# Optimization experiments

Measured on AMD Instinct MI355X. Metric: run time of the kernel, lower is better.

## Reference

```python
import jax, jax.numpy as jnp
import numpy as np

DIM = 2048
N_HEADS = 32
N_KV_HEADS = 8
HEAD_DIM = DIM // N_HEADS  # 64
N_REP = N_HEADS // N_KV_HEADS  # 4
BSZ = 2
SEQ = 2048


def setup_inputs() -> dict:
    key = jax.random.key(0)
    ks = jax.random.split(key, 7)
    s = 0.02
    return {
        "x": jax.random.normal(ks[0], (BSZ, SEQ, DIM), dtype=jnp.float32),
        "freqs_cos": jnp.cos(jnp.outer(jnp.arange(SEQ, dtype=jnp.float32),
                                       1.0 / (10000.0 ** (jnp.arange(0, HEAD_DIM, 2, dtype=jnp.float32) / HEAD_DIM)))),
        "freqs_sin": jnp.sin(jnp.outer(jnp.arange(SEQ, dtype=jnp.float32),
                                       1.0 / (10000.0 ** (jnp.arange(0, HEAD_DIM, 2, dtype=jnp.float32) / HEAD_DIM)))),
        "wq": jax.random.normal(ks[1], (DIM, N_HEADS * HEAD_DIM), dtype=jnp.float32) * s,
        "wk": jax.random.normal(ks[2], (DIM, N_KV_HEADS * HEAD_DIM), dtype=jnp.float32) * s,
        "wv": jax.random.normal(ks[3], (DIM, N_KV_HEADS * HEAD_DIM), dtype=jnp.float32) * s,
        "wo": jax.random.normal(ks[4], (N_HEADS * HEAD_DIM, DIM), dtype=jnp.float32) * s,
    }


def _apply_rope(t, cos, sin):
    # t: [b, s, h, hd]; cos/sin: [s, hd/2] -> broadcast [1, s, 1, hd/2]
    tr = t.reshape(t.shape[:-1] + (HEAD_DIM // 2, 2))
    t_r, t_i = tr[..., 0], tr[..., 1]
    c = cos[None, :, None, :]
    s = sin[None, :, None, :]
    out_r = t_r * c - t_i * s
    out_i = t_r * s + t_i * c
    return jnp.stack([out_r, out_i], axis=-1).reshape(t.shape)


def reference(x, freqs_cos, freqs_sin, wq, wk, wv, wo):
    b, s, _ = x.shape
    xq = (x @ wq).reshape(b, s, N_HEADS, HEAD_DIM)
    xk = (x @ wk).reshape(b, s, N_KV_HEADS, HEAD_DIM)
    xv = (x @ wv).reshape(b, s, N_KV_HEADS, HEAD_DIM)

    xq = _apply_rope(xq, freqs_cos, freqs_sin)
    xk = _apply_rope(xk, freqs_cos, freqs_sin)

    # GQA: group query heads over kv heads instead of materializing repeated KV
    # xq -> [b, kv_heads, n_rep, s, hd]
    q = xq.transpose(0, 2, 1, 3).reshape(b, N_KV_HEADS, N_REP, s, HEAD_DIM)
    k = xk.transpose(0, 2, 1, 3)  # [b, kv, s, hd]
    v = xv.transpose(0, 2, 1, 3)  # [b, kv, s, hd]

    scale = 1.0 / jnp.sqrt(jnp.asarray(HEAD_DIM, dtype=x.dtype))
    scores = jnp.einsum("bgrqd,bgkd->bgrqk", q, k) * scale  # [b,kv,rep,s,s]
    causal = jnp.tril(jnp.ones((s, s), dtype=bool))
    scores = jnp.where(causal[None, None, None], scores, jnp.finfo(scores.dtype).min)
    probs = jax.nn.softmax(scores, axis=-1)
    out = jnp.einsum("bgrqk,bgkd->bgrqd", probs, v)  # [b,kv,rep,s,hd]
    out = out.reshape(b, N_HEADS, s, HEAD_DIM).transpose(0, 2, 1, 3).reshape(b, s, N_HEADS * HEAD_DIM)
    return out @ wo
```

## Files before the change

### kernel.cpp

```cpp
#include <hip/hip_runtime.h>

typedef unsigned short u16;
typedef unsigned int u32;
typedef __bf16 bf16x4 __attribute__((ext_vector_type(4)));
typedef __bf16 bf16x8 __attribute__((ext_vector_type(8)));
typedef float f32x4 __attribute__((ext_vector_type(4)));
typedef u32 u32x2 __attribute__((ext_vector_type(2)));
typedef u32 u32x4 __attribute__((ext_vector_type(4)));
typedef short s16x4 __attribute__((ext_vector_type(4)));

struct __align__(4) U16x2 { u16 x, y; };
struct __align__(8) U16x4 { u16 x, y, z, w; };

#define DEV static __device__ __forceinline__

extern "C" __device__ float __ocml_exp2_f32(float);
#if __has_builtin(__builtin_amdgcn_exp2f)
#define EXP2(x) __builtin_amdgcn_exp2f(x)
#else
#define EXP2(x) __ocml_exp2_f32(x)
#endif

DEV u16 f2bf(float f) {
  __bf16 h = (__bf16)f;
  return __builtin_bit_cast(u16, h);
}
DEV float bf2f(u16 u) { return __uint_as_float(((u32)u) << 16); }
DEV u32 pk2bf(float lo, float hi) { return (u32)f2bf(lo) | ((u32)f2bf(hi) << 16); }

DEV void gload16(const void* g, void* l) {
  __builtin_amdgcn_global_load_lds((const __attribute__((address_space(1))) char*)g,
                                   (__attribute__((address_space(3))) char*)l, 16, 0, 0);
}

DEV f32x4 mfma16(bf16x8 a, bf16x8 b, f32x4 c) {
  return __builtin_amdgcn_mfma_f32_16x16x32_bf16(a, b, c, 0, 0, 0);
}

DEV f32x4 mfma_k16(s16x4 a, s16x4 b, f32x4 c) {
#if __has_builtin(__builtin_amdgcn_mfma_f32_16x16x16bf16_1k)
  return __builtin_amdgcn_mfma_f32_16x16x16bf16_1k(a, b, c, 0, 0, 0);
#else
  f32x4 d;
  asm("v_mfma_f32_16x16x16_bf16 %0, %1, %2, %3"
      : "=v"(d)
      : "v"(a), "v"(b), "0"(c));
  return d;
#endif
}

__global__ __launch_bounds__(256) void cvt_x(const float* __restrict__ x, u16* __restrict__ xb) {
  int i = blockIdx.x * 256 + threadIdx.x;
  float4 v = ((const float4*)x)[i];
  U16x4 o;
  o.x = f2bf(v.x); o.y = f2bf(v.y); o.z = f2bf(v.z); o.w = f2bf(v.w);
  ((U16x4*)xb)[i] = o;
}

__global__ __launch_bounds__(256) void tconv(const float* __restrict__ src, u16* __restrict__ dst,
                                             int C, int nOff, int ldd) {
  __shared__ float t[32][33];
  int bx = blockIdx.x, by = blockIdx.y;
  int tx = threadIdx.x, ty = threadIdx.y;
#pragma unroll
  for (int j = 0; j < 4; ++j)
    t[ty + 8 * j][tx] = src[(size_t)(by * 32 + ty + 8 * j) * C + bx * 32 + tx];
  __syncthreads();
#pragma unroll
  for (int j = 0; j < 4; ++j)
    dst[(size_t)(nOff + bx * 32 + ty + 8 * j) * ldd + by * 32 + tx] = f2bf(t[tx][ty + 8 * j]);
}

__global__ __launch_bounds__(256) void vtrans(const u16* __restrict__ qkv, u16* __restrict__ Vt) {
  __shared__ u16 t[32][33];
  int bx = blockIdx.x, by = blockIdx.y, bz = blockIdx.z;
  int tx = threadIdx.x, ty = threadIdx.y;
  int b = bz >> 3, kh = bz & 7;
  const u16* src = qkv + (size_t)(b * 2048 + bx * 32) * 3072 + 2560 + kh * 64 + by * 32;
#pragma unroll
  for (int j = 0; j < 4; ++j) t[ty + 8 * j][tx] = src[(size_t)(ty + 8 * j) * 3072 + tx];
  __syncthreads();
  u16* dst = Vt + ((size_t)bz * 64 + by * 32) * 2048 + bx * 32;
  int pc = ((tx & 15) >> 2) * 8 + ((tx >> 4) << 2) + (tx & 3);
#pragma unroll
  for (int j = 0; j < 4; ++j) dst[(size_t)(ty + 8 * j) * 2048 + pc] = t[tx][ty + 8 * j];
}

__global__ __launch_bounds__(256) void rope_qk(const u16* __restrict__ qkv,
                                               const float* __restrict__ fc,
                                               const float* __restrict__ fs,
                                               u16* __restrict__ Qo, u16* __restrict__ Ko) {
  int t = blockIdx.x * 256 + threadIdx.x;
  int d2 = t & 31;
  int rest = t >> 5;
  int h40 = rest % 40;
  int bs = rest / 40;
  int s = bs & 2047;
  int b = bs >> 11;
  const u16* src;
  u16* dst;
  float qscale;
  if (h40 < 32) {
    src = qkv + (size_t)bs * 3072 + h40 * 64 + 2 * d2;
    dst = Qo + (((size_t)(b * 32 + h40) * 2048 + s) * 64 + 2 * d2);
    qscale = 0.18033688011112042f;
  } else {
    int kh = h40 - 32;
    src = qkv + (size_t)bs * 3072 + 2048 + kh * 64 + 2 * d2;
    dst = Ko + (((size_t)(b * 8 + kh) * 2048 + s) * 64 + 2 * d2);
    qscale = 1.0f;
  }
  U16x2 v = *(const U16x2*)src;
  float xr = bf2f(v.x), xi = bf2f(v.y);
  float c = fc[s * 32 + d2] * qscale, sn = fs[s * 32 + d2] * qscale;
  U16x2 o;
  o.x = f2bf(xr * c - xi * sn);
  o.y = f2bf(xr * sn + xi * c);
  *(U16x2*)dst = o;
}

template <typename OutT>
__global__ __launch_bounds__(256, 2) void gemm_bt(const u16* __restrict__ A,
                                                  const u16* __restrict__ BT,
                                                  OutT* __restrict__ C,
                                                  int M, int N, int K) {
  __shared__ __align__(16) char smem[65536];
  const int tid = threadIdx.x;
  const int lane = tid & 63;
  const int wm = (tid >> 7) & 1, wn = (tid >> 6) & 1;
  const int tm = blockIdx.y, tn = blockIdx.x;
  const int Kb = K * 2;

  f32x4 acc[4][4];
#pragma unroll
  for (int i = 0; i < 4; ++i)
#pragma unroll
    for (int j = 0; j < 4; ++j) acc[i][j] = (f32x4){0.f, 0.f, 0.f, 0.f};

  const char* Ag = (const char*)A + (size_t)tm * 128 * Kb;
  const char* Bg = (const char*)BT + (size_t)tn * 128 * Kb;

  auto stage = [&](int buf, int t) {
#pragma unroll
    for (int i = 0; i < 4; ++i) {
      int vt = i * 256 + tid;
      int row = vt >> 3;
      int cb = (((vt & 7) << 4) ^ ((row & 7) << 4));
      gload16(Ag + (size_t)row * Kb + t * 128 + cb, smem + buf * 16384 + vt * 16);
      gload16(Bg + (size_t)row * Kb + t * 128 + cb, smem + 32768 + buf * 16384 + vt * 16);
    }
  };

  stage(0, 0);
  int cur = 0;
  const int NT = K >> 6;
  for (int t = 0; t < NT; ++t) {
    __syncthreads();
    if (t + 1 < NT) stage(cur ^ 1, t + 1);
    const char* As = smem + cur * 16384;
    const char* Bs = smem + 32768 + cur * 16384;
#pragma unroll
    for (int ks = 0; ks < 2; ++ks) {
      bf16x8 a[4], b[4];
#pragma unroll
      for (int mf = 0; mf < 4; ++mf) {
        int row = wm * 64 + mf * 16 + (lane & 15);
        int cb = (ks * 64 + ((lane >> 4) << 4)) ^ ((row & 7) << 4);
        a[mf] = *(const bf16x8*)(As + row * 128 + cb);
      }
#pragma unroll
      for (int nf = 0; nf < 4; ++nf) {
        int row = wn * 64 + nf * 16 + (lane & 15);
        int cb = (ks * 64 + ((lane >> 4) << 4)) ^ ((row & 7) << 4);
        b[nf] = *(const bf16x8*)(Bs + row * 128 + cb);
      }
#pragma unroll
      for (int mf = 0; mf < 4; ++mf)
#pragma unroll
        for (int nf = 0; nf < 4; ++nf) acc[mf][nf] = mfma16(a[mf], b[nf], acc[mf][nf]);
    }
    cur ^= 1;
  }
#pragma unroll
  for (int mf = 0; mf < 4; ++mf) {
    int row0 = tm * 128 + wm * 64 + mf * 16 + ((lane >> 4) << 2);
#pragma unroll
    for (int nf = 0; nf < 4; ++nf) {
      int col = tn * 128 + wn * 64 + nf * 16 + (lane & 15);
#pragma unroll
      for (int r = 0; r < 4; ++r) {
        float v = acc[mf][nf][r];
        if constexpr (sizeof(OutT) == 4)
          C[(size_t)(row0 + r) * N + col] = v;
        else
          C[(size_t)(row0 + r) * N + col] = f2bf(v);
      }
    }
  }
}

__global__ __launch_bounds__(128, 4) void attn(const u16* __restrict__ Q,
                                               const u16* __restrict__ Kt,
                                               const u16* __restrict__ Vt,
                                               u16* __restrict__ O) {
  __shared__ __align__(16) char smem[16384];

  const int tid = threadIdx.x, lane = tid & 63, w = tid >> 6;
  const int q15 = lane & 15, g = lane >> 4;
  const int bx = blockIdx.x, h = blockIdx.y, b = blockIdx.z;
  const int kh = h >> 2;
  const int QT0 = 63 - bx, QT1 = bx;

  const char* Qg = (const char*)(Q + ((size_t)(b * 32 + h) * 2048) * 64);
  const char* Kg = (const char*)(Kt + ((size_t)(b * 8 + kh) * 2048 * 64));
  const char* Vg = (const char*)(Vt + ((size_t)(b * 8 + kh) * 64 * 2048));

  bf16x8 qf0[2], qf1[2];
#pragma unroll
  for (int ks = 0; ks < 2; ++ks) {
    int r0 = QT0 * 32 + w * 16 + q15;
    int r1 = QT1 * 32 + w * 16 + q15;
    qf0[ks] = *(const bf16x8*)(Qg + (size_t)r0 * 128 + ks * 64 + (g << 4));
    qf1[ks] = *(const bf16x8*)(Qg + (size_t)r1 * 128 + ks * 64 + (g << 4));
  }

  f32x4 acc0[4], acc1[4];
#pragma unroll
  for (int j = 0; j < 4; ++j) {
    acc0[j] = (f32x4){0.f, 0.f, 0.f, 0.f};
    acc1[j] = (f32x4){0.f, 0.f, 0.f, 0.f};
  }
  float m0 = -1e30f, m1 = -1e30f, l0 = 0.f, l1 = 0.f;
  const f32x4 FZ = (f32x4){0.f, 0.f, 0.f, 0.f};

  auto stageKV = [&](int buf, int kt) {
#pragma unroll
    for (int i = 0; i < 2; ++i) {
      int vt = i * 128 + tid;
      int r = vt >> 3, ck = vt & 7;
      gload16(Kg + (size_t)(kt * 32 + r) * 128 + (((ck ^ r) & 7) << 4),
              smem + buf * 8192 + vt * 16);
      int d = vt >> 2, cv = vt & 3;
      gload16(Vg + (size_t)d * 4096 + kt * 64 + (((cv ^ (d >> 1)) & 3) << 4),
              smem + buf * 8192 + 4096 + vt * 16);
    }
  };

  stageKV(0, 0);
  int cur = 0;
  const int nkt = QT0 + 1;
  for (int kt = 0; kt < nkt; ++kt) {
    __syncthreads();
    if (kt + 1 < nkt) stageKV(cur ^ 1, kt + 1);
    const char* Ks = smem + cur * 8192;
    const char* Vs = smem + cur * 8192 + 4096;
    const bool la = (kt <= QT1);

    bf16x8 kf[2][2];
#pragma unroll
    for (int ks = 0; ks < 2; ++ks)
#pragma unroll
      for (int nf = 0; nf < 2; ++nf) {
        int r = nf * 16 + q15;
        int c = (4 * ks + g) ^ (r & 7);
        kf[ks][nf] = *(const bf16x8*)(Ks + r * 128 + (c << 4));
      }

    f32x4 st0[2], st1[2];
    __builtin_amdgcn_s_setprio(1);
#pragma unroll
    for (int nf = 0; nf < 2; ++nf) {
      st0[nf] = mfma16(kf[0][nf], qf0[0], FZ);
      st0[nf] = mfma16(kf[1][nf], qf0[1], st0[nf]);
    }
    if (la) {
#pragma unroll
      for (int nf = 0; nf < 2; ++nf) {
        st1[nf] = mfma16(kf[0][nf], qf1[0], FZ);
        st1[nf] = mfma16(kf[1][nf], qf1[1], st1[nf]);
      }
    }
    __builtin_amdgcn_s_setprio(0);

    if (kt == QT0) {
      int qg = QT0 * 32 + w * 16 + q15;
#pragma unroll
      for (int nf = 0; nf < 2; ++nf)
#pragma unroll
        for (int r = 0; r < 4; ++r) {
          int kg = kt * 32 + nf * 16 + 4 * g + r;
          if (kg > qg) st0[nf][r] = -1e30f;
        }
    }
    if (la && kt == QT1) {
      int qg = QT1 * 32 + w * 16 + q15;
#pragma unroll
      for (int nf = 0; nf < 2; ++nf)
#pragma unroll
        for (int r = 0; r < 4; ++r) {
          int kg = kt * 32 + nf * 16 + 4 * g + r;
          if (kg > qg) st1[nf][r] = -1e30f;
        }
    }

    s16x4 pa0[2], pa1[2];
#pragma unroll
    for (int t = 0; t < 2; ++t) {
      if (t == 1 && !la) break;
      f32x4* st = (t == 0) ? st0 : st1;
      float& m_r = (t == 0) ? m0 : m1;
      float& l_r = (t == 0) ? l0 : l1;
      f32x4* accT = (t == 0) ? acc0 : acc1;
      s16x4* pa = (t == 0) ? pa0 : pa1;

      float vm = fmaxf(fmaxf(fmaxf(st[0][0], st[0][1]), fmaxf(st[0][2], st[0][3])),
                       fmaxf(fmaxf(st[1][0], st[1][1]), fmaxf(st[1][2], st[1][3])));
      vm = fmaxf(vm, __shfl_xor(vm, 16, 64));
      vm = fmaxf(vm, __shfl_xor(vm, 32, 64));
      const bool resc = !__all(vm - m_r <= 8.0f);
      if (resc) {
        float mn = fmaxf(m_r, vm);
        float cr = EXP2(m_r - mn);
        m_r = mn;
        l_r *= cr;
        float cra[4];
#pragma unroll
        for (int r = 0; r < 4; ++r) cra[r] = __shfl(cr, 4 * g + r, 64);
#pragma unroll
        for (int nfd = 0; nfd < 4; ++nfd)
#pragma unroll
          for (int r = 0; r < 4; ++r) accT[nfd][r] *= cra[r];
      }
      float vs = 0.f;
#pragma unroll
      for (int nf = 0; nf < 2; ++nf) {
        float p0 = EXP2(st[nf][0] - m_r);
        float p1 = EXP2(st[nf][1] - m_r);
        float p2 = EXP2(st[nf][2] - m_r);
        float p3 = EXP2(st[nf][3] - m_r);
        vs += (p0 + p1) + (p2 + p3);
        u32x2 pk;
        pk.x = pk2bf(p0, p1);
        pk.y = pk2bf(p2, p3);
        pa[nf] = __builtin_bit_cast(s16x4, pk);
      }
      vs += __shfl_xor(vs, 16, 64);
      vs += __shfl_xor(vs, 32, 64);
      l_r += vs;
    }

#pragma unroll
    for (int nfd = 0; nfd < 4; ++nfd) {
      int d = nfd * 16 + q15;
      int c = (g ^ (d >> 1)) & 3;
      bf16x8 wv = *(const bf16x8*)(Vs + d * 64 + (c << 4));
      u32x4 W = __builtin_bit_cast(u32x4, wv);
      u32x2 wlo, whi;
      wlo.x = W.x; wlo.y = W.y; whi.x = W.z; whi.y = W.w;
      s16x4 v0 = __builtin_bit_cast(s16x4, wlo);
      s16x4 v1 = __builtin_bit_cast(s16x4, whi);
      __builtin_amdgcn_s_setprio(1);
      acc0[nfd] = mfma_k16(pa0[0], v0, acc0[nfd]);
      acc0[nfd] = mfma_k16(pa0[1], v1, acc0[nfd]);
      if (la) {
        acc1[nfd] = mfma_k16(pa1[0], v0, acc1[nfd]);
        acc1[nfd] = mfma_k16(pa1[1], v1, acc1[nfd]);
      }
      __builtin_amdgcn_s_setprio(0);
    }
    cur ^= 1;
  }

#pragma unroll
  for (int t = 0; t < 2; ++t) {
    float l_r = (t == 0) ? l0 : l1;
    f32x4* accT = (t == 0) ? acc0 : acc1;
    int qt = (t == 0) ? QT0 : QT1;
    u16* Og = O + ((size_t)(b * 2048 + qt * 32 + w * 16) * 2048 + h * 64);
    float la4[4];
#pragma unroll
    for (int r = 0; r < 4; ++r) la4[r] = __shfl(l_r, 4 * g + r, 64);
#pragma unroll
    for (int r = 0; r < 4; ++r) {
      float li = 1.f / la4[r];
#pragma unroll
      for (int nfd = 0; nfd < 4; ++nfd)
        Og[(size_t)(4 * g + r) * 2048 + nfd * 16 + q15] = f2bf(accT[nfd][r] * li);
    }
  }
}

extern "C" void kernel_launch(void* const* d_in, const int* in_sizes, int n_in,
                              void* d_out, int out_size, void* d_ws, size_t ws_size,
                              hipStream_t stream) {
  const float* x = (const float*)d_in[0];
  const float* fc = (const float*)d_in[1];
  const float* fs = (const float*)d_in[2];
  const float* wq = (const float*)d_in[3];
  const float* wk = (const float*)d_in[4];
  const float* wv = (const float*)d_in[5];
  const float* wo = (const float*)d_in[6];
  float* out = (float*)d_out;
  char* ws = (char*)d_ws;

  u16* xb    = (u16*)(ws);
  u16* qkv   = (u16*)(ws + 16777216);
  u16* woT   = (u16*)(ws + 41943040);
  u16* wqkvT = (u16*)(ws + 50331648);
  u16* Kbuf  = (u16*)(ws + 50331648);
  u16* Vtb   = (u16*)(ws + 54525952);
  u16* Qbuf = xb;
  u16* Obuf = qkv;

  dim3 tb(32, 8);
  cvt_x<<<dim3(8192), dim3(256), 0, stream>>>(x, xb);
  tconv<<<dim3(64, 64), tb, 0, stream>>>(wq, wqkvT, 2048, 0, 2048);
  tconv<<<dim3(16, 64), tb, 0, stream>>>(wk, wqkvT, 512, 2048, 2048);
  tconv<<<dim3(16, 64), tb, 0, stream>>>(wv, wqkvT, 512, 2560, 2048);
  tconv<<<dim3(64, 64), tb, 0, stream>>>(wo, woT, 2048, 0, 2048);
  gemm_bt<u16><<<dim3(24, 32), dim3(256), 0, stream>>>(xb, wqkvT, qkv, 4096, 3072, 2048);
  rope_qk<<<dim3(20480), dim3(256), 0, stream>>>(qkv, fc, fs, Qbuf, Kbuf);
  vtrans<<<dim3(64, 2, 16), tb, 0, stream>>>(qkv, Vtb);
  attn<<<dim3(32, 32, 2), dim3(128), 0, stream>>>(Qbuf, Kbuf, Vtb, Obuf);
  gemm_bt<float><<<dim3(16, 32), dim3(256), 0, stream>>>(Obuf, woT, out, 4096, 2048, 2048);
}
```

Measured before the change: 221.3 us.

## Use 16x16x32 bf16 MFMA for PV by permuting K rows and V layout

Replaces the pair of 16x16x16 MFMAs in the P·V product with a single 16x16x32 MFMA per tile. To make the score registers line up with the wider K-dim operand layout, K rows are permuted when staged into shared memory and the V transpose drops its column permutation, with the causal mask indices updated to match. This halves the PV MFMA instruction count and removes register shuffling, at the cost of a more intricate index mapping that must stay consistent across the staging, masking and transpose kernels.

```diff
diff --git a/kernel.cpp b/kernel.cpp
--- a/kernel.cpp
+++ b/kernel.cpp
@@ -5,9 +5,7 @@
 typedef __bf16 bf16x4 __attribute__((ext_vector_type(4)));
 typedef __bf16 bf16x8 __attribute__((ext_vector_type(8)));
 typedef float f32x4 __attribute__((ext_vector_type(4)));
-typedef u32 u32x2 __attribute__((ext_vector_type(2)));
 typedef u32 u32x4 __attribute__((ext_vector_type(4)));
-typedef short s16x4 __attribute__((ext_vector_type(4)));
 
 struct __align__(4) U16x2 { u16 x, y; };
 struct __align__(8) U16x4 { u16 x, y, z, w; };
@@ -37,18 +35,6 @@
   return __builtin_amdgcn_mfma_f32_16x16x32_bf16(a, b, c, 0, 0, 0);
 }
 
-DEV f32x4 mfma_k16(s16x4 a, s16x4 b, f32x4 c) {
-#if __has_builtin(__builtin_amdgcn_mfma_f32_16x16x16bf16_1k)
-  return __builtin_amdgcn_mfma_f32_16x16x16bf16_1k(a, b, c, 0, 0, 0);
-#else
-  f32x4 d;
-  asm("v_mfma_f32_16x16x16_bf16 %0, %1, %2, %3"
-      : "=v"(d)
-      : "v"(a), "v"(b), "0"(c));
-  return d;
-#endif
-}
-
 __global__ __launch_bounds__(256) void cvt_x(const float* __restrict__ x, u16* __restrict__ xb) {
   int i = blockIdx.x * 256 + threadIdx.x;
   float4 v = ((const float4*)x)[i];
@@ -81,9 +67,8 @@
   for (int j = 0; j < 4; ++j) t[ty + 8 * j][tx] = src[(size_t)(ty + 8 * j) * 3072 + tx];
   __syncthreads();
   u16* dst = Vt + ((size_t)bz * 64 + by * 32) * 2048 + bx * 32;
-  int pc = ((tx & 15) >> 2) * 8 + ((tx >> 4) << 2) + (tx & 3);
-#pragma unroll
-  for (int j = 0; j < 4; ++j) dst[(size_t)(ty + 8 * j) * 2048 + pc] = t[tx][ty + 8 * j];
+#pragma unroll
+  for (int j = 0; j < 4; ++j) dst[(size_t)(ty + 8 * j) * 2048 + tx] = t[tx][ty + 8 * j];
 }
 
 __global__ __launch_bounds__(256) void rope_qk(const u16* __restrict__ qkv,
@@ -237,8 +222,9 @@
 #pragma unroll
     for (int i = 0; i < 2; ++i) {
       int vt = i * 128 + tid;
-      int r = vt >> 3, ck = vt & 7;
-      gload16(Kg + (size_t)(kt * 32 + r) * 128 + (((ck ^ r) & 7) << 4),
+      int rho = vt >> 3, ck = vt & 7;
+      int kap = ((rho & 12) << 1) + ((rho & 16) >> 2) + (rho & 3);
+      gload16(Kg + (size_t)(kt * 32 + kap) * 128 + (((ck ^ rho) & 7) << 4),
               smem + buf * 8192 + vt * 16);
       int d = vt >> 2, cv = vt & 3;
       gload16(Vg + (size_t)d * 4096 + kt * 64 + (((cv ^ (d >> 1)) & 3) << 4),
@@ -288,7 +274,7 @@
       for (int nf = 0; nf < 2; ++nf)
 #pragma unroll
         for (int r = 0; r < 4; ++r) {
-          int kg = kt * 32 + nf * 16 + 4 * g + r;
+          int kg = kt * 32 + 8 * g + 4 * nf + r;
           if (kg > qg) st0[nf][r] = -1e30f;
         }
     }
@@ -298,12 +284,12 @@
       for (int nf = 0; nf < 2; ++nf)
 #pragma unroll
         for (int r = 0; r < 4; ++r) {
-          int kg = kt * 32 + nf * 16 + 4 * g + r;
+          int kg = kt * 32 + 8 * g + 4 * nf + r;
           if (kg > qg) st1[nf][r] = -1e30f;
         }
     }
 
-    s16x4 pa0[2], pa1[2];
+    bf16x8 pa0, pa1;
 #pragma unroll
     for (int t = 0; t < 2; ++t) {
       if (t == 1 && !la) break;
@@ -311,7 +297,6 @@
       float& m_r = (t == 0) ? m0 : m1;
       float& l_r = (t == 0) ? l0 : l1;
       f32x4* accT = (t == 0) ? acc0 : acc1;
-      s16x4* pa = (t == 0) ? pa0 : pa1;
 
       float vm = fmaxf(fmaxf(fmaxf(st[0][0], st[0][1]), fmaxf(st[0][2], st[0][3])),
                        fmaxf(fmaxf(st[1][0], st[1][1]), fmaxf(st[1][2], st[1][3])));
@@ -332,18 +317,20 @@
           for (int r = 0; r < 4; ++r) accT[nfd][r] *= cra[r];
       }
       float vs = 0.f;
-#pragma unroll
-      for (int nf = 0; nf < 2; ++nf) {
-        float p0 = EXP2(st[nf][0] - m_r);
-        float p1 = EXP2(st[nf][1] - m_r);
-        float p2 = EXP2(st[nf][2] - m_r);
-        float p3 = EXP2(st[nf][3] - m_r);
-        vs += (p0 + p1) + (p2 + p3);
-        u32x2 pk;
-        pk.x = pk2bf(p0, p1);
-        pk.y = pk2bf(p2, p3);
-        pa[nf] = __builtin_bit_cast(s16x4, pk);
-      }
+      u32x4 W;
+      {
+        float p0 = EXP2(st[0][0] - m_r), p1 = EXP2(st[0][1] - m_r);
+        float p2 = EXP2(st[0][2] - m_r), p3 = EXP2(st[0][3] - m_r);
+        float p4 = EXP2(st[1][0] - m_r), p5 = EXP2(st[1][1] - m_r);
+        float p6 = EXP2(st[1][2] - m_r), p7 = EXP2(st[1][3] - m_r);
+        vs = ((p0 + p1) + (p2 + p3)) + ((p4 + p5) + (p6 + p7));
+        W.x = pk2bf(p0, p1);
+        W.y = pk2bf(p2, p3);
+        W.z = pk2bf(p4, p5);
+        W.w = pk2bf(p6, p7);
+      }
+      if (t == 0) pa0 = __builtin_bit_cast(bf16x8, W);
+      else pa1 = __builtin_bit_cast(bf16x8, W);
       vs += __shfl_xor(vs, 16, 64);
       vs += __shfl_xor(vs, 32, 64);
       l_r += vs;
@@ -353,19 +340,10 @@
     for (int nfd = 0; nfd < 4; ++nfd) {
       int d = nfd * 16 + q15;
       int c = (g ^ (d >> 1)) & 3;
-      bf16x8 wv = *(const bf16x8*)(Vs + d * 64 + (c << 4));
-      u32x4 W = __builtin_bit_cast(u32x4, wv);
-      u32x2 wlo, whi;
-      wlo.x = W.x; wlo.y = W.y; whi.x = W.z; whi.y = W.w;
-      s16x4 v0 = __builtin_bit_cast(s16x4, wlo);
-      s16x4 v1 = __builtin_bit_cast(s16x4, whi);
+      bf16x8 vb = *(const bf16x8*)(Vs + d * 64 + (c << 4));
       __builtin_amdgcn_s_setprio(1);
-      acc0[nfd] = mfma_k16(pa0[0], v0, acc0[nfd]);
-      acc0[nfd] = mfma_k16(pa0[1], v1, acc0[nfd]);
-      if (la) {
-        acc1[nfd] = mfma_k16(pa1[0], v0, acc1[nfd]);
-        acc1[nfd] = mfma_k16(pa1[1], v1, acc1[nfd]);
-      }
+      acc0[nfd] = mfma16(pa0, vb, acc0[nfd]);
+      if (la) acc1[nfd] = mfma16(pa1, vb, acc1[nfd]);
       __builtin_amdgcn_s_setprio(0);
     }
     cur ^= 1;
```

Result: no change. 219.5 us (-0.8%).
